# Kernel optimization log

Hardware: AMD Instinct MI355X
Metric: run time of the kernel (lower is better)

The kernel has to match this reference:

```python
import math
import jax, jax.numpy as jnp
import numpy as np

B, S, H = 8, 2048, 1024
NH = 1
DH = H // NH          # head dim == hidden since NH=1 (required by module's math)
DT = 64               # distance_type


def setup_inputs() -> dict:
    key = jax.random.key(0)
    ks = jax.random.split(key, 10)
    hidden_states = jax.random.normal(ks[0], (B, S, H), dtype=jnp.float32)
    attention_mask = jnp.zeros((B, 1, 1, S), dtype=jnp.float32)
    word_word_relation = jax.random.randint(ks[1], (B, S, S), 0, DT, dtype=jnp.int32)
    init = 0.02
    Wq = jax.random.normal(ks[2], (H, H), dtype=jnp.float32) * init
    bq = jnp.zeros((H,), dtype=jnp.float32)
    Wk = jax.random.normal(ks[3], (H, H), dtype=jnp.float32) * init
    bk = jnp.zeros((H,), dtype=jnp.float32)
    Wv = jax.random.normal(ks[4], (H, H), dtype=jnp.float32) * init
    bv = jnp.zeros((H,), dtype=jnp.float32)
    dist_emb = jax.random.normal(ks[5], (DT, H), dtype=jnp.float32) * init
    dist_emb = dist_emb.at[0].set(0.0)  # padding_idx=0
    return {
        "hidden_states": hidden_states,
        "attention_mask": attention_mask,
        "word_word_relation": word_word_relation,
        "Wq": Wq, "bq": bq, "Wk": Wk, "bk": bk, "Wv": Wv, "bv": bv,
        "dist_emb": dist_emb,
    }


def reference(hidden_states, attention_mask, word_word_relation,
              Wq, bq, Wk, bk, Wv, bv, dist_emb):
    b, s, h = hidden_states.shape
    def heads(x):  # [b,s,h] -> [b,nh,s,dh]
        return x.reshape(b, s, NH, DH).transpose(0, 2, 1, 3)
    q = heads(hidden_states @ Wq.T + bq)
    k = heads(hidden_states @ Wk.T + bk)
    v = heads(hidden_states @ Wv.T + bv)

    scores = jnp.einsum('bhqd,bhkd->bhqk', q, k)                 # [b,nh,s,s]
    word_dot_distance = jnp.einsum('bhqd,td->bhqt', q, dist_emb) # [b,nh,s,DT]

    idx = word_word_relation[:, None, :, :]                      # [b,1,s,s]
    bias = jnp.take_along_axis(word_dot_distance, idx, axis=3)
    mask_out = (word_word_relation == 1)[:, None].astype(scores.dtype)
    bias = bias * mask_out

    scores = (scores + bias) / math.sqrt(DH) + attention_mask
    probs = jax.nn.softmax(scores, axis=-1)
    ctx = jnp.einsum('bhqk,bhkd->bhqd', probs, v)
    ctx = ctx.transpose(0, 2, 1, 3).reshape(b, s, h)
    return ctx
```

## Files before the change

### kernel.cpp

```cpp
#include <hip/hip_runtime.h>

typedef unsigned short u16;
typedef __bf16 bf16x8 __attribute__((ext_vector_type(8)));
typedef u16 u16x8 __attribute__((ext_vector_type(8)));
typedef float f32x4 __attribute__((ext_vector_type(4)));

#define S_LEN 2048
#define H_LEN 1024

__device__ __forceinline__ u16 f2b(float f) {
  unsigned u = __float_as_uint(f);
  return (u16)((u + 0x7FFFu + ((u >> 16) & 1u)) >> 16);
}
__device__ __forceinline__ float b2f(u16 h) { return __uint_as_float(((unsigned)h) << 16); }

#define GLOAD16(gp, lp)                                   \
  __builtin_amdgcn_global_load_lds(                       \
      (__attribute__((address_space(1))) void*)(gp),      \
      (__attribute__((address_space(3))) void*)(lp), 16, 0, 0)

#define FENCE() asm volatile("" ::: "memory")
#define PBAR()                           \
  do {                                   \
    FENCE();                             \
    __builtin_amdgcn_s_barrier();        \
    FENCE();                             \
  } while (0)
#define WAIT_LGKM0()                                        \
  do {                                                      \
    asm volatile("s_waitcnt lgkmcnt(0)" ::: "memory");      \
    __builtin_amdgcn_sched_barrier(0);                      \
  } while (0)
#define WAIT_VM(n) asm volatile("s_waitcnt vmcnt(" #n ")" ::: "memory")

__device__ __forceinline__ f32x4 MM(bf16x8 a, bf16x8 b, f32x4 c) {
  return __builtin_amdgcn_mfma_f32_16x16x32_bf16(a, b, c, 0, 0, 0);
}

__global__ __launch_bounds__(256) void prep_kernel(
    const float* __restrict__ X, const float* __restrict__ Wq,
    const float* __restrict__ Wk, const float* __restrict__ Wv,
    const float* __restrict__ bq, const float* __restrict__ bk,
    const float* __restrict__ bv, const float* __restrict__ dist,
    const int* __restrict__ rel,
    u16* __restrict__ Xbf, u16* __restrict__ Wbf, float* __restrict__ b_all,
    u16* __restrict__ de1, unsigned* __restrict__ bits, float* __restrict__ d1) {
  size_t tid = (size_t)blockIdx.x * blockDim.x + threadIdx.x;
  size_t nth = (size_t)gridDim.x * blockDim.x;
  for (size_t i = tid; i < 4194304u; i += nth) {
    float4 v = ((const float4*)X)[i];
    ushort4 o; o.x = f2b(v.x); o.y = f2b(v.y); o.z = f2b(v.z); o.w = f2b(v.w);
    ((ushort4*)Xbf)[i] = o;
  }
  for (size_t i = tid; i < 786432u; i += nth) {
    int which = (int)(i >> 18);
    size_t off = i & 262143u;
    const float4* src = (const float4*)(which == 0 ? Wq : (which == 1 ? Wk : Wv));
    float4 v = src[off];
    ushort4 o; o.x = f2b(v.x); o.y = f2b(v.y); o.z = f2b(v.z); o.w = f2b(v.w);
    ((ushort4*)Wbf)[i] = o;
  }
  const int4* r4 = (const int4*)rel;
  for (size_t wi = tid; wi < 1048576u; wi += nth) {
    const int4* s = r4 + wi * 8;
    unsigned m = 0;
#pragma unroll
    for (int u = 0; u < 8; ++u) {
      int4 v = s[u];
      m |= (unsigned)(v.x == 1) << (u * 4 + 0);
      m |= (unsigned)(v.y == 1) << (u * 4 + 1);
      m |= (unsigned)(v.z == 1) << (u * 4 + 2);
      m |= (unsigned)(v.w == 1) << (u * 4 + 3);
    }
    bits[wi] = m;
  }
  for (size_t i = tid; i < 256u; i += nth) {
    float4 v = ((const float4*)(dist + H_LEN))[i];
    ushort4 o; o.x = f2b(v.x); o.y = f2b(v.y); o.z = f2b(v.z); o.w = f2b(v.w);
    ((ushort4*)de1)[i] = o;
  }
  for (size_t i = tid; i < 3072u; i += nth)
    b_all[i] = (i < 1024) ? bq[i] : (i < 2048 ? bk[i - 1024] : bv[i - 2048]);
  for (size_t i = tid; i < 32768u; i += nth) d1[i] = 0.f;
}

struct GArgs {
  const u16* A; const u16* B;
  long long sA, sB;
  int ldA, ldB, K;
  u16 *Qo, *Ko, *Vo; const float* b_all; const u16* de1; float* d1;
  const unsigned* relbits; const float* mask; u16* P; float* denom;
  float* outp;
};

template <int EPI>
__global__ __launch_bounds__(512, 2) void gemm256(GArgs g) {
  const int bz = blockIdx.z;
  int bx = blockIdx.x, by = blockIdx.y;
  if constexpr (EPI == 0) {
    const int lin = bx;
    const int wg = (lin & 7) * 96 + (lin >> 3);
    by = wg / 12; bx = wg % 12;
  }
  const u16* Abase = g.A + (size_t)bz * g.sA;
  const u16* Bbase = g.B + (size_t)bz * g.sB;
  const int m0 = by * 256, n0 = bx * 256;

  __shared__ u16 smem[65536];

  const int tid = threadIdx.x;
  const int lane = tid & 63, w = tid >> 6;
  const int wm = w >> 2, wn = w & 3;
  const int l15 = lane & 15, quad = lane >> 4;

  f32x4 acc[8][4];
  const f32x4 zero = {0.f, 0.f, 0.f, 0.f};
#pragma unroll
  for (int a = 0; a < 8; ++a)
#pragma unroll
    for (int b = 0; b < 4; ++b) acc[a][b] = zero;

  const u16* gA[4]; const u16* gB[4]; int qoff[4];
#pragma unroll
  for (int r = 0; r < 4; ++r) {
    const int q = r * 512 + tid;
    const int row = q >> 3, ch = q & 7;
    const int chS = ch ^ (row & 7);
    gA[r] = Abase + (size_t)(m0 + row) * g.ldA + chS * 8;
    gB[r] = Bbase + (size_t)(n0 + row) * g.ldB + chS * 8;
    qoff[r] = q * 8;
  }

  auto stage = [&](int boff2, int kt) {
#pragma unroll
    for (int r = 0; r < 4; ++r) GLOAD16(gA[r] + kt, &smem[boff2 + qoff[r]]);
#pragma unroll
    for (int r = 0; r < 4; ++r) GLOAD16(gB[r] + kt, &smem[boff2 + 16384 + qoff[r]]);
  };

  const int NT = g.K >> 6;

  stage(0, 0);
  stage(32768, 64);
  WAIT_VM(8);
  PBAR();

  bf16x8 af[4][2], bfr[4][2];

  for (int t = 0; t < NT; ++t) {
    const int boff = (t & 1) << 15;
    const u16* Ab = smem + boff;
    const u16* Bb = smem + boff + 16384;

#pragma unroll
    for (int mt = 0; mt < 4; ++mt) {
      const int row = wm * 128 + mt * 16 + l15;
      const int base = row * 64, rx = row & 7;
      af[mt][0] = *(const bf16x8*)&Ab[base + ((quad ^ rx) << 3)];
      af[mt][1] = *(const bf16x8*)&Ab[base + (((quad + 4) ^ rx) << 3)];
    }
#pragma unroll
    for (int nt = 0; nt < 2; ++nt) {
      const int row = wn * 64 + nt * 16 + l15;
      const int base = row * 64, rx = row & 7;
      bfr[nt][0] = *(const bf16x8*)&Bb[base + ((quad ^ rx) << 3)];
      bfr[nt][1] = *(const bf16x8*)&Bb[base + (((quad + 4) ^ rx) << 3)];
    }
    PBAR();
    WAIT_LGKM0();
    __builtin_amdgcn_s_setprio(1);
#pragma unroll
    for (int mt = 0; mt < 4; ++mt)
#pragma unroll
      for (int nt = 0; nt < 2; ++nt) {
        acc[mt][nt] = MM(af[mt][0], bfr[nt][0], acc[mt][nt]);
        acc[mt][nt] = MM(af[mt][1], bfr[nt][1], acc[mt][nt]);
      }
    __builtin_amdgcn_s_setprio(0);
    PBAR();

#pragma unroll
    for (int nt = 2; nt < 4; ++nt) {
      const int row = wn * 64 + nt * 16 + l15;
      const int base = row * 64, rx = row & 7;
      bfr[nt][0] = *(const bf16x8*)&Bb[base + ((quad ^ rx) << 3)];
      bfr[nt][1] = *(const bf16x8*)&Bb[base + (((quad + 4) ^ rx) << 3)];
    }
    PBAR();
    WAIT_LGKM0();
    __builtin_amdgcn_s_setprio(1);
#pragma unroll
    for (int mt = 0; mt < 4; ++mt)
#pragma unroll
      for (int nt = 2; nt < 4; ++nt) {
        acc[mt][nt] = MM(af[mt][0], bfr[nt][0], acc[mt][nt]);
        acc[mt][nt] = MM(af[mt][1], bfr[nt][1], acc[mt][nt]);
      }
    __builtin_amdgcn_s_setprio(0);
    PBAR();

#pragma unroll
    for (int mt = 0; mt < 4; ++mt) {
      const int row = wm * 128 + (mt + 4) * 16 + l15;
      const int base = row * 64, rx = row & 7;
      af[mt][0] = *(const bf16x8*)&Ab[base + ((quad ^ rx) << 3)];
      af[mt][1] = *(const bf16x8*)&Ab[base + (((quad + 4) ^ rx) << 3)];
    }
    PBAR();
    WAIT_LGKM0();
    __builtin_amdgcn_s_setprio(1);
#pragma unroll
    for (int mt = 0; mt < 4; ++mt)
#pragma unroll
      for (int nt = 0; nt < 2; ++nt) {
        acc[mt + 4][nt] = MM(af[mt][0], bfr[nt][0], acc[mt + 4][nt]);
        acc[mt + 4][nt] = MM(af[mt][1], bfr[nt][1], acc[mt + 4][nt]);
      }
    __builtin_amdgcn_s_setprio(0);
    PBAR();

    if (t + 2 < NT) stage(boff, (t + 2) << 6);
    PBAR();
    WAIT_LGKM0();
    __builtin_amdgcn_s_setprio(1);
#pragma unroll
    for (int mt = 0; mt < 4; ++mt)
#pragma unroll
      for (int nt = 2; nt < 4; ++nt) {
        acc[mt + 4][nt] = MM(af[mt][0], bfr[nt][0], acc[mt + 4][nt]);
        acc[mt + 4][nt] = MM(af[mt][1], bfr[nt][1], acc[mt + 4][nt]);
      }
    __builtin_amdgcn_s_setprio(0);
    if (t + 2 < NT) {
      WAIT_VM(8);
    } else if (t + 1 < NT) {
      WAIT_VM(0);
    }
    PBAR();
  }

  const int nbase = n0 + wn * 64;

  if constexpr (EPI == 0) {
    const int which = n0 >> 10;
    const int nl0 = n0 & 1023;
    float bv4[4], dw[4];
#pragma unroll
    for (int nt = 0; nt < 4; ++nt) {
      const int col = wn * 64 + nt * 16 + l15;
      bv4[nt] = g.b_all[n0 + col];
      dw[nt] = (which == 0) ? b2f(g.de1[nl0 + col]) : 0.f;
    }
#pragma unroll
    for (int mt = 0; mt < 8; ++mt)
#pragma unroll
      for (int r = 0; r < 4; ++r) {
        const int row = wm * 128 + mt * 16 + quad * 4 + r;
        float part = 0.f;
#pragma unroll
        for (int nt = 0; nt < 4; ++nt) {
          const float v = acc[mt][nt][r] + bv4[nt];
          part += v * dw[nt];
          const int col = wn * 64 + nt * 16 + l15;
          const int chS = (col >> 3) ^ (row & 31);
          smem[row * 256 + chS * 8 + (col & 7)] = f2b(v);
        }
        if (which == 0) {
          part += __shfl_xor(part, 1);
          part += __shfl_xor(part, 2);
          part += __shfl_xor(part, 4);
          part += __shfl_xor(part, 8);
          if (l15 == 0) atomicAdd(&g.d1[m0 + row], part);
        }
      }
    __syncthreads();
    u16* dstbuf = which == 0 ? g.Qo : (which == 1 ? g.Ko : g.Vo);
#pragma unroll
    for (int p = 0; p < 16; ++p) {
      const int flat = p * 512 + tid;
      const int row = flat >> 5, chunk = flat & 31;
      const int chS = chunk ^ (row & 31);
      u16x8 v = *(const u16x8*)&smem[row * 256 + chS * 8];
      *(u16x8*)(dstbuf + (size_t)(m0 + row) * H_LEN + nl0 + chunk * 8) = v;
    }
  }

  if constexpr (EPI == 1) {
    float mk[4];
#pragma unroll
    for (int nt = 0; nt < 4; ++nt) mk[nt] = g.mask[bz * S_LEN + nbase + nt * 16 + l15];
    const size_t bSS = (size_t)bz * S_LEN * S_LEN;
    const int wbase = (n0 + wn * 64) >> 5;
#pragma unroll
    for (int mt = 0; mt < 8; ++mt)
#pragma unroll
      for (int r = 0; r < 4; ++r) {
        const int row = wm * 128 + mt * 16 + quad * 4 + r;
        const int gi = bz * S_LEN + m0 + row;
        const float d1v = g.d1[gi] * 0.03125f;
        const unsigned w0 = g.relbits[(size_t)gi * 64 + wbase];
        const unsigned w1 = g.relbits[(size_t)gi * 64 + wbase + 1];
        float dsum = 0.f;
#pragma unroll
        for (int nt = 0; nt < 4; ++nt) {
          const unsigned word = (nt & 2) ? w1 : w0;
          const int pos = (nt * 16 + l15) & 31;
          const float bias = ((word >> pos) & 1) ? d1v : 0.f;
          const float logit = acc[mt][nt][r] * 0.03125f + bias + mk[nt];
          const float pv = __expf(logit);
          const u16 pb = f2b(pv);
          dsum += b2f(pb);
          const int col = wn * 64 + nt * 16 + l15;
          const int chS = (col >> 3) ^ (row & 31);
          smem[row * 256 + chS * 8 + (col & 7)] = pb;
        }
        dsum += __shfl_xor(dsum, 1);
        dsum += __shfl_xor(dsum, 2);
        dsum += __shfl_xor(dsum, 4);
        dsum += __shfl_xor(dsum, 8);
        if (l15 == 0) atomicAdd(&g.denom[gi], dsum);
      }
    __syncthreads();
#pragma unroll
    for (int p = 0; p < 16; ++p) {
      const int flat = p * 512 + tid;
      const int row = flat >> 5, chunk = flat & 31;
      const int chS = chunk ^ (row & 31);
      u16x8 v = *(const u16x8*)&smem[row * 256 + chS * 8];
      *(u16x8*)(g.P + bSS + (size_t)(m0 + row) * S_LEN + n0 + chunk * 8) = v;
    }
  }

  if constexpr (EPI == 2) {
    const size_t ob = (size_t)bz * S_LEN * H_LEN;
#pragma unroll
    for (int mt = 0; mt < 8; ++mt)
#pragma unroll
      for (int r = 0; r < 4; ++r) {
        const int row = wm * 128 + mt * 16 + quad * 4 + r;
        const float inv = 1.0f / g.denom[bz * S_LEN + m0 + row];
        const size_t rowo = ob + (size_t)(m0 + row) * H_LEN;
#pragma unroll
        for (int nt = 0; nt < 4; ++nt)
          g.outp[rowo + nbase + nt * 16 + l15] = acc[mt][nt][r] * inv;
      }
  }
}

__global__ __launch_bounds__(256) void transpose_v(const u16* __restrict__ V,
                                                   u16* __restrict__ Vt) {
  const int b = blockIdx.z;
  const int j0 = blockIdx.x * 64;
  const int d0 = blockIdx.y * 64;
  __shared__ u16 t[64][72];
  const int tid = threadIdx.x;
  const int tr = tid >> 4;
  const int tc = (tid & 15) * 4;
#pragma unroll
  for (int p = 0; p < 4; ++p) {
    const int jl = p * 16 + tr;
    const u16* src = V + ((size_t)b * S_LEN + (j0 + jl)) * H_LEN + d0 + tc;
    ushort4 v = *(const ushort4*)src;
    t[jl][tc + 0] = v.x; t[jl][tc + 1] = v.y; t[jl][tc + 2] = v.z; t[jl][tc + 3] = v.w;
  }
  __syncthreads();
#pragma unroll
  for (int p = 0; p < 4; ++p) {
    const int dl = p * 16 + tr;
    ushort4 v;
    v.x = t[tc + 0][dl]; v.y = t[tc + 1][dl]; v.z = t[tc + 2][dl]; v.w = t[tc + 3][dl];
    *(ushort4*)(Vt + ((size_t)b * H_LEN + (d0 + dl)) * S_LEN + j0 + tc) = v;
  }
}

extern "C" void kernel_launch(void* const* d_in, const int* in_sizes, int n_in,
                              void* d_out, int out_size, void* d_ws, size_t ws_size,
                              hipStream_t stream) {
  (void)in_sizes; (void)n_in; (void)out_size; (void)ws_size;
  const float* X    = (const float*)d_in[0];
  const float* mask = (const float*)d_in[1];
  const int*   rel  = (const int*)d_in[2];
  const float* Wq   = (const float*)d_in[3];
  const float* bq   = (const float*)d_in[4];
  const float* Wk   = (const float*)d_in[5];
  const float* bk   = (const float*)d_in[6];
  const float* Wv   = (const float*)d_in[7];
  const float* bv   = (const float*)d_in[8];
  const float* dist = (const float*)d_in[9];
  float* out = (float*)d_out;

  char* p = (char*)d_ws;
  u16* Xbf = (u16*)p;      p += (size_t)16384 * 1024 * 2;
  u16* Wbf = (u16*)p;      p += (size_t)3072 * 1024 * 2;
  float* b_all = (float*)p; p += 3072 * 4;
  u16* de1 = (u16*)p;      p += 4096;
  u16* Qb = (u16*)p;       p += (size_t)16384 * 1024 * 2;
  u16* Kb = (u16*)p;       p += (size_t)16384 * 1024 * 2;
  u16* Vb = (u16*)p;       p += (size_t)16384 * 1024 * 2;
  u16* Vt = (u16*)p;       p += (size_t)16384 * 1024 * 2;
  float* d1 = (float*)p;   p += 16384 * 4;
  float* denom = (float*)p; p += 16384 * 4;
  unsigned* relbits = (unsigned*)p; p += (size_t)1048576 * 4;
  u16* P = (u16*)p;        p += (size_t)8 * 2048 * 2048 * 2;

  prep_kernel<<<1024, 256, 0, stream>>>(X, Wq, Wk, Wv, bq, bk, bv, dist, rel,
                                        Xbf, Wbf, b_all, de1, relbits, d1);

  GArgs g0 = {};
  g0.A = Xbf; g0.B = Wbf; g0.sA = 0; g0.sB = 0;
  g0.ldA = 1024; g0.ldB = 1024; g0.K = 1024;
  g0.Qo = Qb; g0.Ko = Kb; g0.Vo = Vb; g0.b_all = b_all; g0.de1 = de1; g0.d1 = d1;
  gemm256<0><<<dim3(768, 1, 1), dim3(512, 1, 1), 0, stream>>>(g0);

  transpose_v<<<dim3(32, 16, 8), dim3(256, 1, 1), 0, stream>>>(Vb, Vt);

  GArgs g1 = {};
  g1.A = Qb; g1.B = Kb; g1.sA = 2048LL * 1024; g1.sB = 2048LL * 1024;
  g1.ldA = 1024; g1.ldB = 1024; g1.K = 1024;
  g1.relbits = relbits; g1.d1 = d1; g1.mask = mask; g1.P = P; g1.denom = denom;
  gemm256<1><<<dim3(8, 8, 8), dim3(512, 1, 1), 0, stream>>>(g1);

  GArgs g2 = {};
  g2.A = P; g2.B = Vt; g2.sA = 2048LL * 2048; g2.sB = 1024LL * 2048;
  g2.ldA = 2048; g2.ldB = 2048; g2.K = 2048;
  g2.denom = denom; g2.outp = out;
  gemm256<2><<<dim3(4, 8, 8), dim3(512, 1, 1), 0, stream>>>(g2);
}
```

Measured before the change: 611.7 us.

## Preload all LDS fragments per k-tile and remap GEMM blocks by XCD

Each k-tile's inner loop now loads all A and B fragments from LDS up front into separate register sets, then issues the four MFMA groups back-to-back. This removes the intermediate barriers and LDS waits between groups and moves the next-tile prefetch before the last group. The QK and PV GEMMs now launch on a 1D grid with an XCD-aware swizzle, so consecutive blocks on the same XCD share a batch and row tiles for L2 reuse. Holding more fragments raises register pressure under launch_bounds(512,2), which could cause spills.

Result: faster. 592.3 us (-3.2%).

```diff
diff --git a/kernel.cpp b/kernel.cpp
--- a/kernel.cpp
+++ b/kernel.cpp
@@ -95,12 +95,19 @@
 
 template <int EPI>
 __global__ __launch_bounds__(512, 2) void gemm256(GArgs g) {
-  const int bz = blockIdx.z;
-  int bx = blockIdx.x, by = blockIdx.y;
-  if constexpr (EPI == 0) {
-    const int lin = bx;
-    const int wg = (lin & 7) * 96 + (lin >> 3);
-    by = wg / 12; bx = wg % 12;
+  int bx, by, bz;
+  {
+    const int lin = blockIdx.x;
+    if constexpr (EPI == 0) {
+      const int wg = (lin & 7) * 96 + (lin >> 3);
+      by = wg / 12; bx = wg % 12; bz = 0;
+    } else if constexpr (EPI == 1) {
+      const int wg = (lin & 7) * 64 + (lin >> 3);
+      bz = wg >> 6; by = (wg >> 3) & 7; bx = wg & 7;
+    } else {
+      const int wg = (lin & 7) * 32 + (lin >> 3);
+      bz = wg >> 5; by = (wg >> 2) & 7; bx = wg & 3;
+    }
   }
   const u16* Abase = g.A + (size_t)bz * g.sA;
   const u16* Bbase = g.B + (size_t)bz * g.sB;
@@ -145,7 +152,7 @@
   WAIT_VM(8);
   PBAR();
 
-  bf16x8 af[4][2], bfr[4][2];
+  bf16x8 af0[4][2], af1[4][2], bf0[2][2], bf1[2][2];
 
   for (int t = 0; t < NT; ++t) {
     const int boff = (t & 1) << 15;
@@ -156,81 +163,87 @@
     for (int mt = 0; mt < 4; ++mt) {
       const int row = wm * 128 + mt * 16 + l15;
       const int base = row * 64, rx = row & 7;
-      af[mt][0] = *(const bf16x8*)&Ab[base + ((quad ^ rx) << 3)];
-      af[mt][1] = *(const bf16x8*)&Ab[base + (((quad + 4) ^ rx) << 3)];
+      af0[mt][0] = *(const bf16x8*)&Ab[base + ((quad ^ rx) << 3)];
+      af0[mt][1] = *(const bf16x8*)&Ab[base + (((quad + 4) ^ rx) << 3)];
     }
 #pragma unroll
     for (int nt = 0; nt < 2; ++nt) {
       const int row = wn * 64 + nt * 16 + l15;
       const int base = row * 64, rx = row & 7;
-      bfr[nt][0] = *(const bf16x8*)&Bb[base + ((quad ^ rx) << 3)];
-      bfr[nt][1] = *(const bf16x8*)&Bb[base + (((quad + 4) ^ rx) << 3)];
-    }
-    PBAR();
-    WAIT_LGKM0();
-    __builtin_amdgcn_s_setprio(1);
-#pragma unroll
-    for (int mt = 0; mt < 4; ++mt)
-#pragma unroll
-      for (int nt = 0; nt < 2; ++nt) {
-        acc[mt][nt] = MM(af[mt][0], bfr[nt][0], acc[mt][nt]);
-        acc[mt][nt] = MM(af[mt][1], bfr[nt][1], acc[mt][nt]);
-      }
-    __builtin_amdgcn_s_setprio(0);
-    PBAR();
-
-#pragma unroll
-    for (int nt = 2; nt < 4; ++nt) {
-      const int row = wn * 64 + nt * 16 + l15;
+      bf0[nt][0] = *(const bf16x8*)&Bb[base + ((quad ^ rx) << 3)];
+      bf0[nt][1] = *(const bf16x8*)&Bb[base + (((quad + 4) ^ rx) << 3)];
+    }
+#pragma unroll
+    for (int nt = 0; nt < 2; ++nt) {
+      const int row = wn * 64 + (nt + 2) * 16 + l15;
       const int base = row * 64, rx = row & 7;
-      bfr[nt][0] = *(const bf16x8*)&Bb[base + ((quad ^ rx) << 3)];
-      bfr[nt][1] = *(const bf16x8*)&Bb[base + (((quad + 4) ^ rx) << 3)];
-    }
-    PBAR();
-    WAIT_LGKM0();
-    __builtin_amdgcn_s_setprio(1);
-#pragma unroll
-    for (int mt = 0; mt < 4; ++mt)
-#pragma unroll
-      for (int nt = 2; nt < 4; ++nt) {
-        acc[mt][nt] = MM(af[mt][0], bfr[nt][0], acc[mt][nt]);
-        acc[mt][nt] = MM(af[mt][1], bfr[nt][1], acc[mt][nt]);
-      }
-    __builtin_amdgcn_s_setprio(0);
-    PBAR();
-
+      bf1[nt][0] = *(const bf16x8*)&Bb[base + ((quad ^ rx) << 3)];
+      bf1[nt][1] = *(const bf16x8*)&Bb[base + (((quad + 4) ^ rx) << 3)];
+    }
 #pragma unroll
     for (int mt = 0; mt < 4; ++mt) {
       const int row = wm * 128 + (mt + 4) * 16 + l15;
       const int base = row * 64, rx = row & 7;
-      af[mt][0] = *(const bf16x8*)&Ab[base + ((quad ^ rx) << 3)];
-      af[mt][1] = *(const bf16x8*)&Ab[base + (((quad + 4) ^ rx) << 3)];
-    }
+      af1[mt][0] = *(const bf16x8*)&Ab[base + ((quad ^ rx) << 3)];
+      af1[mt][1] = *(const bf16x8*)&Ab[base + (((quad + 4) ^ rx) << 3)];
+    }
+
+    __builtin_amdgcn_s_setprio(1);
+#pragma unroll
+    for (int mt = 0; mt < 4; ++mt)
+#pragma unroll
+      for (int nt = 0; nt < 2; ++nt)
+        acc[mt][nt] = MM(af0[mt][0], bf0[nt][0], acc[mt][nt]);
+#pragma unroll
+    for (int mt = 0; mt < 4; ++mt)
+#pragma unroll
+      for (int nt = 0; nt < 2; ++nt)
+        acc[mt][nt] = MM(af0[mt][1], bf0[nt][1], acc[mt][nt]);
+    __builtin_amdgcn_s_setprio(0);
+
+    __builtin_amdgcn_s_setprio(1);
+#pragma unroll
+    for (int mt = 0; mt < 4; ++mt)
+#pragma unroll
+      for (int nt = 0; nt < 2; ++nt)
+        acc[mt][nt + 2] = MM(af0[mt][0], bf1[nt][0], acc[mt][nt + 2]);
+#pragma unroll
+    for (int mt = 0; mt < 4; ++mt)
+#pragma unroll
+      for (int nt = 0; nt < 2; ++nt)
+        acc[mt][nt + 2] = MM(af0[mt][1], bf1[nt][1], acc[mt][nt + 2]);
+    __builtin_amdgcn_s_setprio(0);
+
+    __builtin_amdgcn_s_setprio(1);
+#pragma unroll
+    for (int mt = 0; mt < 4; ++mt)
+#pragma unroll
+      for (int nt = 0; nt < 2; ++nt)
+        acc[mt + 4][nt] = MM(af1[mt][0], bf0[nt][0], acc[mt + 4][nt]);
+#pragma unroll
+    for (int mt = 0; mt < 4; ++mt)
+#pragma unroll
+      for (int nt = 0; nt < 2; ++nt)
+        acc[mt + 4][nt] = MM(af1[mt][1], bf0[nt][1], acc[mt + 4][nt]);
+    __builtin_amdgcn_s_setprio(0);
+
+    WAIT_LGKM0();
     PBAR();
-    WAIT_LGKM0();
+    if (t + 2 < NT) stage(boff, (t + 2) << 6);
+
     __builtin_amdgcn_s_setprio(1);
 #pragma unroll
     for (int mt = 0; mt < 4; ++mt)
 #pragma unroll
-      for (int nt = 0; nt < 2; ++nt) {
-        acc[mt + 4][nt] = MM(af[mt][0], bfr[nt][0], acc[mt + 4][nt]);
-        acc[mt + 4][nt] = MM(af[mt][1], bfr[nt][1], acc[mt + 4][nt]);
-      }
+      for (int nt = 0; nt < 2; ++nt)
+        acc[mt + 4][nt + 2] = MM(af1[mt][0], bf1[nt][0], acc[mt + 4][nt + 2]);
+#pragma unroll
+    for (int mt = 0; mt < 4; ++mt)
+#pragma unroll
+      for (int nt = 0; nt < 2; ++nt)
+        acc[mt + 4][nt + 2] = MM(af1[mt][1], bf1[nt][1], acc[mt + 4][nt + 2]);
     __builtin_amdgcn_s_setprio(0);
-    PBAR();
-
-    if (t + 2 < NT) stage(boff, (t + 2) << 6);
-    PBAR();
-    WAIT_LGKM0();
-    __builtin_amdgcn_s_setprio(1);
-#pragma unroll
-    for (int mt = 0; mt < 4; ++mt)
-#pragma unroll
-      for (int nt = 2; nt < 4; ++nt) {
-        acc[mt + 4][nt] = MM(af[mt][0], bfr[nt][0], acc[mt + 4][nt]);
-        acc[mt + 4][nt] = MM(af[mt][1], bfr[nt][1], acc[mt + 4][nt]);
-      }
-    __builtin_amdgcn_s_setprio(0);
+
     if (t + 2 < NT) {
       WAIT_VM(8);
     } else if (t + 1 < NT) {
@@ -418,11 +431,11 @@
   g1.A = Qb; g1.B = Kb; g1.sA = 2048LL * 1024; g1.sB = 2048LL * 1024;
   g1.ldA = 1024; g1.ldB = 1024; g1.K = 1024;
   g1.relbits = relbits; g1.d1 = d1; g1.mask = mask; g1.P = P; g1.denom = denom;
-  gemm256<1><<<dim3(8, 8, 8), dim3(512, 1, 1), 0, stream>>>(g1);
+  gemm256<1><<<dim3(512, 1, 1), dim3(512, 1, 1), 0, stream>>>(g1);
 
   GArgs g2 = {};
   g2.A = P; g2.B = Vt; g2.sA = 2048LL * 2048; g2.sB = 1024LL * 2048;
   g2.ldA = 2048; g2.ldB = 2048; g2.K = 2048;
   g2.denom = denom; g2.outp = out;
-  gemm256<2><<<dim3(4, 8, 8), dim3(512, 1, 1), 0, stream>>>(g2);
-}
+  gemm256<2><<<dim3(256, 1, 1), dim3(512, 1, 1), 0, stream>>>(g2);
+}
```
